# Kernel tuning notes

Hardware: AMD Instinct MI355X
Metric: run time of the kernel (lower is better)

Reference implementation:

```python
import jax, jax.numpy as jnp
import numpy as np

NEG_INF = -1e10
DIST_THRESH = 0


def _collect_entities(rep, pos, mask):
    # rep: [B, N, H]; pos: [B, M, S] int; mask: [B, M, S] float
    B, M, S = pos.shape
    g = jnp.take_along_axis(rep, pos.reshape(B, M * S)[:, :, None], axis=1)  # [B, M*S, H]
    g = g.reshape(B, M, S, rep.shape[-1]) * mask[..., None]
    return g.sum(axis=2)  # [B, M, H]


def setup_inputs() -> dict:
    key = jax.random.key(0)
    ks = jax.random.split(key, 10)
    B, N, H = 8, 2048, 512
    M, S = 96, 16
    E, D, R, MAXD = 256, 64, 5, 600
    scale = 0.02
    return {
        'node_hidden': jax.random.normal(ks[0], (B, N, H), jnp.float32),
        'chem_map': jax.random.randint(ks[1], (B, M, S), 0, N),
        'chem_mask': jnp.ones((B, M, S), jnp.float32),
        'dis_map': jax.random.randint(ks[2], (B, M, S), 0, N),
        'dis_mask': jnp.ones((B, M, S), jnp.float32),
        'distance': jax.random.randint(ks[3], (B, M, M), 0, MAXD),
        'W_chem': jax.random.normal(ks[4], (H, E), jnp.float32) * scale,
        'b_chem': jnp.zeros((E,), jnp.float32),
        'W_dis': jax.random.normal(ks[5], (H, E), jnp.float32) * scale,
        'b_dis': jnp.zeros((E,), jnp.float32),
        'W_score': jax.random.normal(ks[6], (2 * E + H + D, R), jnp.float32) * scale,
        'b_score': jnp.zeros((R,), jnp.float32),
        'dist_emb': jax.random.normal(ks[7], (MAXD, D), jnp.float32) * scale,
    }


def reference(node_hidden, chem_map, chem_mask, dis_map, dis_mask, distance,
              W_chem, b_chem, W_dis, b_dis, W_score, b_score, dist_emb):
    B, M = chem_map.shape[0], chem_map.shape[1]
    E = W_chem.shape[1]

    # sentence representation: max-pool over tokens  -> [B, H]
    sent = jnp.max(node_hidden, axis=1)

    # gather mention spans, masked sum pool, tanh-linear  -> [B, M, E]
    chem = jnp.tanh(_collect_entities(node_hidden, chem_map, chem_mask) @ W_chem + b_chem)
    dis = jnp.tanh(_collect_entities(node_hidden, dis_map, dis_mask) @ W_dis + b_dis)

    dist_e = dist_emb[distance]  # [B, M, M, D]

    # pairwise concat: [chem_i, dis_j, dist_ij, sent]  -> [B, M, M, 2E+D+H]
    concat = jnp.concatenate([
        jnp.broadcast_to(chem[:, :, None, :], (B, M, M, E)),
        jnp.broadcast_to(dis[:, None, :, :], (B, M, M, E)),
        dist_e,
        jnp.broadcast_to(sent[:, None, None, :], (B, M, M, sent.shape[-1])),
    ], axis=-1)

    score = jnp.einsum('bmnf,fr->bmnr', concat, W_score) + b_score  # [B, M, M, R]

    # validity masks: non-empty spans and distance >= threshold
    chem_valid = chem_mask.sum(axis=-1) > 0  # [B, M]
    dis_valid = dis_mask.sum(axis=-1) > 0    # [B, M]
    pair_valid = chem_valid[:, :, None] & dis_valid[:, None, :]  # [B, M, M]
    valid = pair_valid & (distance >= DIST_THRESH)
    score = jnp.where(valid[..., None], score, NEG_INF)

    # max-pool over all mention pairs  -> [B, R]
    return jnp.max(score.reshape(B, M * M, -1), axis=1)
```

## Files before the change

### kernel.cpp

```cpp
#include <hip/hip_runtime.h>
#include <math.h>

constexpr int B = 8, N = 2048, H = 512, M = 96, S = 16;
constexpr int E = 256, D = 64, R = 5, MAXD = 600;
constexpr int NZ = 32;
constexpr int NCHUNK = N / NZ;
constexpr int MT = 8;
constexpr int HC = 4;
constexpr int HCH = H / HC;
constexpr int MT4 = 8;
constexpr int RS = 2 * B * M;
constexpr float NEG_INF = -1e10f;

constexpr int G_GEMM = 2 * B * (M / MT) * HC;
constexpr int G_SENT = B * NZ / 2;
constexpr int G_DIST = MAXD / 4;
constexpr int G1 = G_GEMM + G_SENT + G_DIST;

constexpr int G3_PROJ = RS / 4;
constexpr int G3 = G3_PROJ + B;

__device__ inline void atomicMaxFloat(float* addr, float val) {
    int* ai = (int*)addr;
    int old = *ai;
    while (__int_as_float(old) < val) {
        int assumed = old;
        old = atomicCAS(ai, assumed, __float_as_int(val));
        if (old == assumed) break;
    }
}

__global__ __launch_bounds__(256)
void k1(const float* __restrict__ node,
        const int* __restrict__ cmap, const float* __restrict__ cmask,
        const int* __restrict__ dmap, const float* __restrict__ dmask,
        const float* __restrict__ Wc, const float* __restrict__ Wd,
        const float* __restrict__ Wsc, const float* __restrict__ emb,
        float* __restrict__ part, float* __restrict__ dotp,
        float* __restrict__ validAB, float* __restrict__ sD,
        float* __restrict__ out) {
    const int blk = blockIdx.x;
    const int t = threadIdx.x;

    if (blk == 0 && t < B * R) out[t] = NEG_INF;

    if (blk < G_GEMM) {
        int hc   = blk & 3;
        int rest = blk >> 2;
        int mg = rest % (M / MT);
        int b  = (rest / (M / MT)) % B;
        int z  = rest / ((M / MT) * B);
        const float* W    = z ? Wd : Wc;
        const int*   map  = z ? dmap  : cmap;
        const float* mask = z ? dmask : cmask;

        __shared__ int   smap[MT][S];
        __shared__ float smask[MT][S];
        __shared__ float lp[MT][HCH];

        if (t < MT * S) {
            int mi = t >> 4, s = t & 15;
            size_t off = ((size_t)b * M + mg * MT + mi) * S + s;
            smap[mi][s]  = map[off];
            smask[mi][s] = mask[off];
        }
        __syncthreads();

        {
            int mi = t >> 5, slot = t & 31;
            float4 a = make_float4(0.f, 0.f, 0.f, 0.f);
            #pragma unroll
            for (int s = 0; s < S; ++s) {
                float mk = smask[mi][s];
                const float4 v = reinterpret_cast<const float4*>(
                    node + ((size_t)b * N + smap[mi][s]) * H + hc * HCH)[slot];
                a.x += mk * v.x; a.y += mk * v.y;
                a.z += mk * v.z; a.w += mk * v.w;
            }
            reinterpret_cast<float4*>(&lp[mi][0])[slot] = a;
        }
        if (hc == 0 && t < MT) {
            float ms = 0.f;
            #pragma unroll
            for (int s = 0; s < S; ++s) ms += smask[t][s];
            validAB[((size_t)z * B + b) * M + mg * MT + t] = (ms > 0.f) ? 1.f : 0.f;
        }
        __syncthreads();

        float acc[MT] = {};
        const float* Wp = W + (size_t)(hc * HCH) * E + t;
        #pragma unroll 4
        for (int hh = 0; hh < HCH; hh += 4) {
            float w0 = Wp[(size_t)(hh + 0) * E];
            float w1 = Wp[(size_t)(hh + 1) * E];
            float w2 = Wp[(size_t)(hh + 2) * E];
            float w3 = Wp[(size_t)(hh + 3) * E];
            #pragma unroll
            for (int mi = 0; mi < MT; ++mi) {
                const float4 pv = *reinterpret_cast<const float4*>(&lp[mi][hh]);
                acc[mi] += pv.x * w0 + pv.y * w1 + pv.z * w2 + pv.w * w3;
            }
        }
        #pragma unroll
        for (int mi = 0; mi < MT; ++mi) {
            size_t row = ((size_t)z * B + b) * M + mg * MT + mi;
            dotp[((size_t)hc * RS + row) * E + t] = acc[mi];
        }
    } else if (blk < G_GEMM + G_SENT) {
        int sb = blk - G_GEMM;
        int b = sb >> 4;
        int z = ((sb & 15) << 1) + (t >> 7);
        int tt = t & 127;
        const float4* p = reinterpret_cast<const float4*>(
            node + ((size_t)b * N + (size_t)z * NCHUNK) * H) + tt;
        float4 mx = p[0];
        #pragma unroll 8
        for (int n = 1; n < NCHUNK; ++n) {
            float4 v = p[(size_t)n * (H / 4)];
            mx.x = fmaxf(mx.x, v.x); mx.y = fmaxf(mx.y, v.y);
            mx.z = fmaxf(mx.z, v.z); mx.w = fmaxf(mx.w, v.w);
        }
        reinterpret_cast<float4*>(part + ((size_t)z * B + b) * H)[tt] = mx;
    } else {
        int d = (blk - G_GEMM - G_SENT) * 4 + (t >> 6);
        int k = t & 63;
        float v = emb[(size_t)d * D + k];
        #pragma unroll
        for (int r = 0; r < R; ++r) {
            float p = v * Wsc[(size_t)(2 * E + k) * R + r];
            for (int off = 32; off; off >>= 1) p += __shfl_down(p, off, 64);
            if (k == 0) sD[d * R + r] = p;
        }
    }
}

__global__ __launch_bounds__(256)
void k3(const float* __restrict__ dotp,
        const float* __restrict__ bc, const float* __restrict__ bd,
        const float* __restrict__ Wsc, const float* __restrict__ bsc,
        const float* __restrict__ part,
        float* __restrict__ sAB, float* __restrict__ sS) {
    const int blk = blockIdx.x;
    const int t = threadIdx.x;
    const int wave = t >> 6, lane = t & 63;

    if (blk < G3_PROJ) {
        int rid = blk * 4 + wave;
        int z = rid / (B * M);
        const float* bias = z ? bd : bc;
        int scoff = z ? E : 0;

        float4 dv = reinterpret_cast<const float4*>(bias)[lane];
        #pragma unroll
        for (int hc = 0; hc < HC; ++hc) {
            const float4 v = reinterpret_cast<const float4*>(
                dotp + ((size_t)hc * RS + rid) * E)[lane];
            dv.x += v.x; dv.y += v.y; dv.z += v.z; dv.w += v.w;
        }
        float v0 = tanhf(dv.x), v1 = tanhf(dv.y), v2 = tanhf(dv.z), v3 = tanhf(dv.w);

        int e0 = scoff + 4 * lane;
        float p[R];
        #pragma unroll
        for (int r = 0; r < R; ++r) {
            p[r] = v0 * Wsc[(size_t)(e0 + 0) * R + r] + v1 * Wsc[(size_t)(e0 + 1) * R + r]
                 + v2 * Wsc[(size_t)(e0 + 2) * R + r] + v3 * Wsc[(size_t)(e0 + 3) * R + r];
        }
        #pragma unroll
        for (int r = 0; r < R; ++r) {
            for (int off = 32; off; off >>= 1) p[r] += __shfl_down(p[r], off, 64);
        }
        if (lane == 0) {
            #pragma unroll
            for (int r = 0; r < R; ++r) sAB[(size_t)rid * R + r] = p[r];
        }
    } else {
        int b = blk - G3_PROJ;
        __shared__ float sent[H];
        __shared__ float red[R][4];
        for (int h = t; h < H; h += 256) {
            float mx = -INFINITY;
            #pragma unroll 8
            for (int z = 0; z < NZ; ++z) mx = fmaxf(mx, part[((size_t)z * B + b) * H + h]);
            sent[h] = mx;
        }
        __syncthreads();
        float acc[R] = {};
        for (int h = t; h < H; h += 256) {
            float v = sent[h];
            const float* w = Wsc + (size_t)(2 * E + D + h) * R;
            #pragma unroll
            for (int r = 0; r < R; ++r) acc[r] += v * w[r];
        }
        #pragma unroll
        for (int r = 0; r < R; ++r) {
            float v = acc[r];
            for (int off = 32; off; off >>= 1) v += __shfl_down(v, off, 64);
            if (lane == 0) red[r][wave] = v;
        }
        __syncthreads();
        if (t < R) sS[b * R + t] = red[t][0] + red[t][1] + red[t][2] + red[t][3] + bsc[t];
    }
}

__global__ __launch_bounds__(256)
void k4(const int* __restrict__ distance,
        const float* __restrict__ sAB, const float* __restrict__ validAB,
        const float* __restrict__ sD, const float* __restrict__ sS,
        float* __restrict__ out) {
    const int g = blockIdx.x % (M / MT4);
    const int b = blockIdx.x / (M / MT4);
    const int t = threadIdx.x;
    const int wave = t >> 6, lane = t & 63;

    __shared__ float lB[M * R];
    __shared__ float lD[MAXD * R];
    __shared__ float lA[MT4 * R];
    __shared__ float lvA[MT4], lvB[M];
    __shared__ float red[R][4];

    for (int i = t; i < M * R; i += 256) lB[i] = sAB[((size_t)(B + b)) * M * R + i];
    for (int i = t; i < MAXD * R; i += 256) lD[i] = sD[i];
    if (t < MT4 * R) lA[t] = sAB[((size_t)b * M + g * MT4) * R + t] + sS[b * R + (t % R)];
    if (t < MT4) lvA[t] = validAB[(size_t)b * M + g * MT4 + t];
    for (int i = t; i < M; i += 256) lvB[i] = validAB[((size_t)B + b) * M + i];
    __syncthreads();

    float mx[R];
    #pragma unroll
    for (int r = 0; r < R; ++r) mx[r] = NEG_INF;

    #pragma unroll
    for (int it = 0; it < (MT4 * M) / 256; ++it) {
        int idx = it * 256 + t;
        int mi = idx / M, n = idx % M;
        int dist = distance[((size_t)b * M + g * MT4 + mi) * M + n];
        if (lvA[mi] > 0.f && lvB[n] > 0.f && dist >= 0 ) {
            #pragma unroll
            for (int r = 0; r < R; ++r)
                mx[r] = fmaxf(mx[r], lA[mi * R + r] + lB[n * R + r] + lD[dist * R + r]);
        }
    }
    #pragma unroll
    for (int r = 0; r < R; ++r) {
        float v = mx[r];
        for (int off = 32; off; off >>= 1) v = fmaxf(v, __shfl_down(v, off, 64));
        if (lane == 0) red[r][wave] = v;
    }
    __syncthreads();
    if (t < R) {
        float v = fmaxf(fmaxf(red[t][0], red[t][1]), fmaxf(red[t][2], red[t][3]));
        atomicMaxFloat(out + b * R + t, v);
    }
}

extern "C" void kernel_launch(void* const* d_in, const int* in_sizes, int n_in,
                              void* d_out, int out_size, void* d_ws, size_t ws_size,
                              hipStream_t stream) {
    const float* node     = (const float*)d_in[0];
    const int*   cmap     = (const int*)  d_in[1];
    const float* cmask    = (const float*)d_in[2];
    const int*   dmap     = (const int*)  d_in[3];
    const float* dmask    = (const float*)d_in[4];
    const int*   distance = (const int*)  d_in[5];
    const float* Wc       = (const float*)d_in[6];
    const float* bc       = (const float*)d_in[7];
    const float* Wd       = (const float*)d_in[8];
    const float* bd       = (const float*)d_in[9];
    const float* Wsc      = (const float*)d_in[10];
    const float* bsc      = (const float*)d_in[11];
    const float* emb      = (const float*)d_in[12];
    float* out = (float*)d_out;

    float* ws      = (float*)d_ws;
    float* part    = ws;
    float* validAB = part + (size_t)NZ * B * H;
    float* sD      = validAB + 2 * B * M;
    float* sS      = sD + MAXD * R;
    float* sAB     = sS + B * R;
    float* dotp    = sAB + (size_t)RS * R;

    hipLaunchKernelGGL(k1, dim3(G1), dim3(256), 0, stream,
                       node, cmap, cmask, dmap, dmask, Wc, Wd, Wsc, emb,
                       part, dotp, validAB, sD, out);
    hipLaunchKernelGGL(k3, dim3(G3), dim3(256), 0, stream,
                       dotp, bc, bd, Wsc, bsc, part, sAB, sS);
    hipLaunchKernelGGL(k4, dim3((M / MT4) * B), dim3(256), 0, stream,
                       distance, sAB, validAB, sD, sS, out);
}
```

Before: 50.43 us.

## Fuse three kernels into one cooperative persistent kernel with grid syncs

Merges the three stage kernels into a single cooperative kernel. Each block loops over work items for each phase, and grid.sync() separates the phases, so two kernel launch boundaries go away. The grid size is taken from an occupancy query, and the old three-launch path is kept as a fallback if the cooperative launch fails. The cost is grid-wide barrier latency, a host-side occupancy query on every call, and possibly lower occupancy, because the kernel's shared memory is the union of all three phases.

```diff
diff --git a/kernel.cpp b/kernel.cpp
--- a/kernel.cpp
+++ b/kernel.cpp
@@ -1,5 +1,8 @@
 #include <hip/hip_runtime.h>
+#include <hip/hip_cooperative_groups.h>
 #include <math.h>
+
+namespace cg = cooperative_groups;
 
 constexpr int B = 8, N = 2048, H = 512, M = 96, S = 16;
 constexpr int E = 256, D = 64, R = 5, MAXD = 600;
@@ -15,10 +18,11 @@
 constexpr int G_GEMM = 2 * B * (M / MT) * HC;
 constexpr int G_SENT = B * NZ / 2;
 constexpr int G_DIST = MAXD / 4;
-constexpr int G1 = G_GEMM + G_SENT + G_DIST;
+constexpr int P1_ITEMS = G_GEMM + G_SENT + G_DIST;
 
 constexpr int G3_PROJ = RS / 4;
-constexpr int G3 = G3_PROJ + B;
+constexpr int P2_ITEMS = G3_PROJ + B;
+constexpr int P3_ITEMS = (M / MT4) * B;
 
 __device__ inline void atomicMaxFloat(float* addr, float val) {
     int* ai = (int*)addr;
@@ -30,33 +34,25 @@
     }
 }
 
-__global__ __launch_bounds__(256)
-void k1(const float* __restrict__ node,
+__device__ __forceinline__ void p1_body(
+        int item, int t,
+        const float* __restrict__ node,
         const int* __restrict__ cmap, const float* __restrict__ cmask,
         const int* __restrict__ dmap, const float* __restrict__ dmask,
         const float* __restrict__ Wc, const float* __restrict__ Wd,
         const float* __restrict__ Wsc, const float* __restrict__ emb,
         float* __restrict__ part, float* __restrict__ dotp,
         float* __restrict__ validAB, float* __restrict__ sD,
-        float* __restrict__ out) {
-    const int blk = blockIdx.x;
-    const int t = threadIdx.x;
-
-    if (blk == 0 && t < B * R) out[t] = NEG_INF;
-
-    if (blk < G_GEMM) {
-        int hc   = blk & 3;
-        int rest = blk >> 2;
+        int smap[MT][S], float smask[MT][S], float lp[MT][HCH]) {
+    if (item < G_GEMM) {
+        int hc   = item & 3;
+        int rest = item >> 2;
         int mg = rest % (M / MT);
         int b  = (rest / (M / MT)) % B;
         int z  = rest / ((M / MT) * B);
         const float* W    = z ? Wd : Wc;
         const int*   map  = z ? dmap  : cmap;
         const float* mask = z ? dmask : cmask;
-
-        __shared__ int   smap[MT][S];
-        __shared__ float smask[MT][S];
-        __shared__ float lp[MT][HCH];
 
         if (t < MT * S) {
             int mi = t >> 4, s = t & 15;
@@ -106,8 +102,8 @@
             size_t row = ((size_t)z * B + b) * M + mg * MT + mi;
             dotp[((size_t)hc * RS + row) * E + t] = acc[mi];
         }
-    } else if (blk < G_GEMM + G_SENT) {
-        int sb = blk - G_GEMM;
+    } else if (item < G_GEMM + G_SENT) {
+        int sb = item - G_GEMM;
         int b = sb >> 4;
         int z = ((sb & 15) << 1) + (t >> 7);
         int tt = t & 127;
@@ -122,7 +118,7 @@
         }
         reinterpret_cast<float4*>(part + ((size_t)z * B + b) * H)[tt] = mx;
     } else {
-        int d = (blk - G_GEMM - G_SENT) * 4 + (t >> 6);
+        int d = (item - G_GEMM - G_SENT) * 4 + (t >> 6);
         int k = t & 63;
         float v = emb[(size_t)d * D + k];
         #pragma unroll
@@ -132,6 +128,184 @@
             if (k == 0) sD[d * R + r] = p;
         }
     }
+}
+
+__device__ __forceinline__ void p2_body(
+        int item, int t,
+        const float* __restrict__ dotp,
+        const float* __restrict__ bc, const float* __restrict__ bd,
+        const float* __restrict__ Wsc, const float* __restrict__ bsc,
+        const float* __restrict__ part,
+        float* __restrict__ sAB, float* __restrict__ sS,
+        float sent[H], float red[R][4]) {
+    const int wave = t >> 6, lane = t & 63;
+    if (item < G3_PROJ) {
+        int rid = item * 4 + wave;
+        int z = rid / (B * M);
+        const float* bias = z ? bd : bc;
+        int scoff = z ? E : 0;
+
+        float4 dv = reinterpret_cast<const float4*>(bias)[lane];
+        #pragma unroll
+        for (int hc = 0; hc < HC; ++hc) {
+            const float4 v = reinterpret_cast<const float4*>(
+                dotp + ((size_t)hc * RS + rid) * E)[lane];
+            dv.x += v.x; dv.y += v.y; dv.z += v.z; dv.w += v.w;
+        }
+        float v0 = tanhf(dv.x), v1 = tanhf(dv.y), v2 = tanhf(dv.z), v3 = tanhf(dv.w);
+
+        int e0 = scoff + 4 * lane;
+        float p[R];
+        #pragma unroll
+        for (int r = 0; r < R; ++r) {
+            p[r] = v0 * Wsc[(size_t)(e0 + 0) * R + r] + v1 * Wsc[(size_t)(e0 + 1) * R + r]
+                 + v2 * Wsc[(size_t)(e0 + 2) * R + r] + v3 * Wsc[(size_t)(e0 + 3) * R + r];
+        }
+        #pragma unroll
+        for (int r = 0; r < R; ++r) {
+            for (int off = 32; off; off >>= 1) p[r] += __shfl_down(p[r], off, 64);
+        }
+        if (lane == 0) {
+            #pragma unroll
+            for (int r = 0; r < R; ++r) sAB[(size_t)rid * R + r] = p[r];
+        }
+    } else {
+        int b = item - G3_PROJ;
+        for (int h = t; h < H; h += 256) {
+            float mx = -INFINITY;
+            #pragma unroll 8
+            for (int z = 0; z < NZ; ++z) mx = fmaxf(mx, part[((size_t)z * B + b) * H + h]);
+            sent[h] = mx;
+        }
+        __syncthreads();
+        float acc[R] = {};
+        for (int h = t; h < H; h += 256) {
+            float v = sent[h];
+            const float* w = Wsc + (size_t)(2 * E + D + h) * R;
+            #pragma unroll
+            for (int r = 0; r < R; ++r) acc[r] += v * w[r];
+        }
+        #pragma unroll
+        for (int r = 0; r < R; ++r) {
+            float v = acc[r];
+            for (int off = 32; off; off >>= 1) v += __shfl_down(v, off, 64);
+            if (lane == 0) red[r][wave] = v;
+        }
+        __syncthreads();
+        if (t < R) sS[b * R + t] = red[t][0] + red[t][1] + red[t][2] + red[t][3] + bsc[t];
+    }
+}
+
+__device__ __forceinline__ void p3_body(
+        int item, int t,
+        const int* __restrict__ distance,
+        const float* __restrict__ sAB, const float* __restrict__ validAB,
+        const float* __restrict__ sD, const float* __restrict__ sS,
+        float* __restrict__ out,
+        float lB[M * R], float lD[MAXD * R], float lA[MT4 * R],
+        float lvA[MT4], float lvB[M], float red[R][4]) {
+    const int g = item % (M / MT4);
+    const int b = item / (M / MT4);
+    const int wave = t >> 6, lane = t & 63;
+
+    for (int i = t; i < M * R; i += 256) lB[i] = sAB[((size_t)(B + b)) * M * R + i];
+    for (int i = t; i < MAXD * R; i += 256) lD[i] = sD[i];
+    if (t < MT4 * R) lA[t] = sAB[((size_t)b * M + g * MT4) * R + t] + sS[b * R + (t % R)];
+    if (t < MT4) lvA[t] = validAB[(size_t)b * M + g * MT4 + t];
+    for (int i = t; i < M; i += 256) lvB[i] = validAB[((size_t)B + b) * M + i];
+    __syncthreads();
+
+    float mx[R];
+    #pragma unroll
+    for (int r = 0; r < R; ++r) mx[r] = NEG_INF;
+
+    #pragma unroll
+    for (int it = 0; it < (MT4 * M) / 256; ++it) {
+        int idx = it * 256 + t;
+        int mi = idx / M, n = idx % M;
+        int dist = distance[((size_t)b * M + g * MT4 + mi) * M + n];
+        if (lvA[mi] > 0.f && lvB[n] > 0.f && dist >= 0 ) {
+            #pragma unroll
+            for (int r = 0; r < R; ++r)
+                mx[r] = fmaxf(mx[r], lA[mi * R + r] + lB[n * R + r] + lD[dist * R + r]);
+        }
+    }
+    #pragma unroll
+    for (int r = 0; r < R; ++r) {
+        float v = mx[r];
+        for (int off = 32; off; off >>= 1) v = fmaxf(v, __shfl_down(v, off, 64));
+        if (lane == 0) red[r][wave] = v;
+    }
+    __syncthreads();
+    if (t < R) {
+        float v = fmaxf(fmaxf(red[t][0], red[t][1]), fmaxf(red[t][2], red[t][3]));
+        atomicMaxFloat(out + b * R + t, v);
+    }
+}
+
+__global__ __launch_bounds__(256, 4)
+void k_coop(const float* __restrict__ node,
+            const int* __restrict__ cmap, const float* __restrict__ cmask,
+            const int* __restrict__ dmap, const float* __restrict__ dmask,
+            const int* __restrict__ distance,
+            const float* __restrict__ Wc, const float* __restrict__ bc,
+            const float* __restrict__ Wd, const float* __restrict__ bd,
+            const float* __restrict__ Wsc, const float* __restrict__ bsc,
+            const float* __restrict__ emb,
+            float* __restrict__ part, float* __restrict__ dotp,
+            float* __restrict__ validAB, float* __restrict__ sD,
+            float* __restrict__ sAB, float* __restrict__ sS,
+            float* __restrict__ out) {
+    cg::grid_group grid = cg::this_grid();
+    const int t = threadIdx.x;
+    const int blk = blockIdx.x;
+    const int GD = gridDim.x;
+
+    __shared__ int   smap[MT][S];
+    __shared__ float smask[MT][S];
+    __shared__ float lp[MT][HCH];
+    __shared__ float sent[H];
+    __shared__ float red[R][4];
+    __shared__ float lB[M * R];
+    __shared__ float lD[MAXD * R];
+    __shared__ float lA[MT4 * R];
+    __shared__ float lvA[MT4], lvB[M];
+
+    if (blk == 0 && t < B * R) out[t] = NEG_INF;
+
+    for (int item = blk; item < P1_ITEMS; item += GD) {
+        __syncthreads();
+        p1_body(item, t, node, cmap, cmask, dmap, dmask, Wc, Wd, Wsc, emb,
+                part, dotp, validAB, sD, smap, smask, lp);
+    }
+    grid.sync();
+    for (int item = blk; item < P2_ITEMS; item += GD) {
+        __syncthreads();
+        p2_body(item, t, dotp, bc, bd, Wsc, bsc, part, sAB, sS, sent, red);
+    }
+    grid.sync();
+    for (int item = blk; item < P3_ITEMS; item += GD) {
+        __syncthreads();
+        p3_body(item, t, distance, sAB, validAB, sD, sS, out,
+                lB, lD, lA, lvA, lvB, red);
+    }
+}
+
+__global__ __launch_bounds__(256)
+void k1(const float* __restrict__ node,
+        const int* __restrict__ cmap, const float* __restrict__ cmask,
+        const int* __restrict__ dmap, const float* __restrict__ dmask,
+        const float* __restrict__ Wc, const float* __restrict__ Wd,
+        const float* __restrict__ Wsc, const float* __restrict__ emb,
+        float* __restrict__ part, float* __restrict__ dotp,
+        float* __restrict__ validAB, float* __restrict__ sD,
+        float* __restrict__ out) {
+    __shared__ int   smap[MT][S];
+    __shared__ float smask[MT][S];
+    __shared__ float lp[MT][HCH];
+    if (blockIdx.x == 0 && threadIdx.x < B * R) out[threadIdx.x] = NEG_INF;
+    p1_body(blockIdx.x, threadIdx.x, node, cmap, cmask, dmap, dmask, Wc, Wd, Wsc, emb,
+            part, dotp, validAB, sD, smap, smask, lp);
 }
 
 __global__ __launch_bounds__(256)
@@ -140,67 +314,9 @@
         const float* __restrict__ Wsc, const float* __restrict__ bsc,
         const float* __restrict__ part,
         float* __restrict__ sAB, float* __restrict__ sS) {
-    const int blk = blockIdx.x;
-    const int t = threadIdx.x;
-    const int wave = t >> 6, lane = t & 63;
-
-    if (blk < G3_PROJ) {
-        int rid = blk * 4 + wave;
-        int z = rid / (B * M);
-        const float* bias = z ? bd : bc;
-        int scoff = z ? E : 0;
-
-        float4 dv = reinterpret_cast<const float4*>(bias)[lane];
-        #pragma unroll
-        for (int hc = 0; hc < HC; ++hc) {
-            const float4 v = reinterpret_cast<const float4*>(
-                dotp + ((size_t)hc * RS + rid) * E)[lane];
-            dv.x += v.x; dv.y += v.y; dv.z += v.z; dv.w += v.w;
-        }
-        float v0 = tanhf(dv.x), v1 = tanhf(dv.y), v2 = tanhf(dv.z), v3 = tanhf(dv.w);
-
-        int e0 = scoff + 4 * lane;
-        float p[R];
-        #pragma unroll
-        for (int r = 0; r < R; ++r) {
-            p[r] = v0 * Wsc[(size_t)(e0 + 0) * R + r] + v1 * Wsc[(size_t)(e0 + 1) * R + r]
-                 + v2 * Wsc[(size_t)(e0 + 2) * R + r] + v3 * Wsc[(size_t)(e0 + 3) * R + r];
-        }
-        #pragma unroll
-        for (int r = 0; r < R; ++r) {
-            for (int off = 32; off; off >>= 1) p[r] += __shfl_down(p[r], off, 64);
-        }
-        if (lane == 0) {
-            #pragma unroll
-            for (int r = 0; r < R; ++r) sAB[(size_t)rid * R + r] = p[r];
-        }
-    } else {
-        int b = blk - G3_PROJ;
-        __shared__ float sent[H];
-        __shared__ float red[R][4];
-        for (int h = t; h < H; h += 256) {
-            float mx = -INFINITY;
-            #pragma unroll 8
-            for (int z = 0; z < NZ; ++z) mx = fmaxf(mx, part[((size_t)z * B + b) * H + h]);
-            sent[h] = mx;
-        }
-        __syncthreads();
-        float acc[R] = {};
-        for (int h = t; h < H; h += 256) {
-            float v = sent[h];
-            const float* w = Wsc + (size_t)(2 * E + D + h) * R;
-            #pragma unroll
-            for (int r = 0; r < R; ++r) acc[r] += v * w[r];
-        }
-        #pragma unroll
-        for (int r = 0; r < R; ++r) {
-            float v = acc[r];
-            for (int off = 32; off; off >>= 1) v += __shfl_down(v, off, 64);
-            if (lane == 0) red[r][wave] = v;
-        }
-        __syncthreads();
-        if (t < R) sS[b * R + t] = red[t][0] + red[t][1] + red[t][2] + red[t][3] + bsc[t];
-    }
+    __shared__ float sent[H];
+    __shared__ float red[R][4];
+    p2_body(blockIdx.x, threadIdx.x, dotp, bc, bd, Wsc, bsc, part, sAB, sS, sent, red);
 }
 
 __global__ __launch_bounds__(256)
@@ -208,50 +324,13 @@
         const float* __restrict__ sAB, const float* __restrict__ validAB,
         const float* __restrict__ sD, const float* __restrict__ sS,
         float* __restrict__ out) {
-    const int g = blockIdx.x % (M / MT4);
-    const int b = blockIdx.x / (M / MT4);
-    const int t = threadIdx.x;
-    const int wave = t >> 6, lane = t & 63;
-
     __shared__ float lB[M * R];
     __shared__ float lD[MAXD * R];
     __shared__ float lA[MT4 * R];
     __shared__ float lvA[MT4], lvB[M];
     __shared__ float red[R][4];
-
-    for (int i = t; i < M * R; i += 256) lB[i] = sAB[((size_t)(B + b)) * M * R + i];
-    for (int i = t; i < MAXD * R; i += 256) lD[i] = sD[i];
-    if (t < MT4 * R) lA[t] = sAB[((size_t)b * M + g * MT4) * R + t] + sS[b * R + (t % R)];
-    if (t < MT4) lvA[t] = validAB[(size_t)b * M + g * MT4 + t];
-    for (int i = t; i < M; i += 256) lvB[i] = validAB[((size_t)B + b) * M + i];
-    __syncthreads();
-
-    float mx[R];
-    #pragma unroll
-    for (int r = 0; r < R; ++r) mx[r] = NEG_INF;
-
-    #pragma unroll
-    for (int it = 0; it < (MT4 * M) / 256; ++it) {
-        int idx = it * 256 + t;
-        int mi = idx / M, n = idx % M;
-        int dist = distance[((size_t)b * M + g * MT4 + mi) * M + n];
-        if (lvA[mi] > 0.f && lvB[n] > 0.f && dist >= 0 ) {
-            #pragma unroll
-            for (int r = 0; r < R; ++r)
-                mx[r] = fmaxf(mx[r], lA[mi * R + r] + lB[n * R + r] + lD[dist * R + r]);
-        }
-    }
-    #pragma unroll
-    for (int r = 0; r < R; ++r) {
-        float v = mx[r];
-        for (int off = 32; off; off >>= 1) v = fmaxf(v, __shfl_down(v, off, 64));
-        if (lane == 0) red[r][wave] = v;
-    }
-    __syncthreads();
-    if (t < R) {
-        float v = fmaxf(fmaxf(red[t][0], red[t][1]), fmaxf(red[t][2], red[t][3]));
-        atomicMaxFloat(out + b * R + t, v);
-    }
+    p3_body(blockIdx.x, threadIdx.x, distance, sAB, validAB, sD, sS, out,
+            lB, lD, lA, lvA, lvB, red);
 }
 
 extern "C" void kernel_launch(void* const* d_in, const int* in_sizes, int n_in,
@@ -280,11 +359,29 @@
     float* sAB     = sS + B * R;
     float* dotp    = sAB + (size_t)RS * R;
 
-    hipLaunchKernelGGL(k1, dim3(G1), dim3(256), 0, stream,
-                       node, cmap, cmask, dmap, dmask, Wc, Wd, Wsc, emb,
-                       part, dotp, validAB, sD, out);
-    hipLaunchKernelGGL(k3, dim3(G3), dim3(256), 0, stream,
-                       dotp, bc, bd, Wsc, bsc, part, sAB, sS);
-    hipLaunchKernelGGL(k4, dim3((M / MT4) * B), dim3(256), 0, stream,
-                       distance, sAB, validAB, sD, sS, out);
-}
+    int occ = 0;
+    hipError_t qerr = hipOccupancyMaxActiveBlocksPerMultiprocessor(&occ, k_coop, 256, 0);
+    int grid = occ * 256;
+    if (grid > 1024) grid = 1024;
+
+    hipError_t lerr = hipErrorUnknown;
+    if (qerr == hipSuccess && grid >= 128) {
+        void* args[] = {
+            (void*)&node, (void*)&cmap, (void*)&cmask, (void*)&dmap, (void*)&dmask,
+            (void*)&distance, (void*)&Wc, (void*)&bc, (void*)&Wd, (void*)&bd,
+            (void*)&Wsc, (void*)&bsc, (void*)&emb,
+            (void*)&part, (void*)&dotp, (void*)&validAB, (void*)&sD,
+            (void*)&sAB, (void*)&sS, (void*)&out
+        };
+        lerr = hipLaunchCooperativeKernel((void*)k_coop, dim3(grid), dim3(256), args, 0, stream);
+    }
+    if (lerr != hipSuccess) {
+        hipLaunchKernelGGL(k1, dim3(P1_ITEMS), dim3(256), 0, stream,
+                           node, cmap, cmask, dmap, dmask, Wc, Wd, Wsc, emb,
+                           part, dotp, validAB, sD, out);
+        hipLaunchKernelGGL(k3, dim3(P2_ITEMS), dim3(256), 0, stream,
+                           dotp, bc, bd, Wsc, bsc, part, sAB, sS);
+        hipLaunchKernelGGL(k4, dim3(P3_ITEMS), dim3(256), 0, stream,
+                           distance, sAB, validAB, sD, sS, out);
+    }
+}
```

Result: slower. 196.1 us (+288.9%).

## Fuse entity projection epilogue into gather-GEMM and sentence score into pair-max kernel

Applied to the files above, without the earlier changes.

The separate projection-reduction kernel is removed. Each GEMM block now handles 4 mentions with all four H-chunks split across waves, reduces the partials in shared memory, and applies the bias, tanh and score projection in place. The sentence max and its score are computed redundantly inside each pair-max block, so the pipeline goes from three launches to two and the dotp workspace round trip disappears. In exchange, each GEMM block reads the full W with float4 loads (fewer blocks, more work per block), and every pair-max block re-reduces the 32 partial sentence maxima.

```diff
diff --git a/kernel.cpp b/kernel.cpp
--- a/kernel.cpp
+++ b/kernel.cpp
@@ -5,20 +5,16 @@
 constexpr int E = 256, D = 64, R = 5, MAXD = 600;
 constexpr int NZ = 32;
 constexpr int NCHUNK = N / NZ;
-constexpr int MT = 8;
+constexpr int MT = 4;
 constexpr int HC = 4;
 constexpr int HCH = H / HC;
 constexpr int MT4 = 8;
-constexpr int RS = 2 * B * M;
 constexpr float NEG_INF = -1e10f;
 
-constexpr int G_GEMM = 2 * B * (M / MT) * HC;
-constexpr int G_SENT = B * NZ / 2;
-constexpr int G_DIST = MAXD / 4;
-constexpr int G1 = G_GEMM + G_SENT + G_DIST;
-
-constexpr int G3_PROJ = RS / 4;
-constexpr int G3 = G3_PROJ + B;
+constexpr int X_GEMM = 2 * B * (M / MT);
+constexpr int X_SENT = B * NZ / 2;
+constexpr int X_DIST = MAXD / 4;
+constexpr int XG = X_GEMM + X_SENT + X_DIST;
 
 __device__ inline void atomicMaxFloat(float* addr, float val) {
     int* ai = (int*)addr;
@@ -31,32 +27,35 @@
 }
 
 __global__ __launch_bounds__(256)
-void k1(const float* __restrict__ node,
+void kX(const float* __restrict__ node,
         const int* __restrict__ cmap, const float* __restrict__ cmask,
         const int* __restrict__ dmap, const float* __restrict__ dmask,
-        const float* __restrict__ Wc, const float* __restrict__ Wd,
+        const float* __restrict__ Wc, const float* __restrict__ bc,
+        const float* __restrict__ Wd, const float* __restrict__ bd,
         const float* __restrict__ Wsc, const float* __restrict__ emb,
-        float* __restrict__ part, float* __restrict__ dotp,
+        float* __restrict__ part, float* __restrict__ sAB,
         float* __restrict__ validAB, float* __restrict__ sD,
         float* __restrict__ out) {
     const int blk = blockIdx.x;
     const int t = threadIdx.x;
+    const int wave = t >> 6, lane = t & 63;
 
     if (blk == 0 && t < B * R) out[t] = NEG_INF;
 
-    if (blk < G_GEMM) {
-        int hc   = blk & 3;
-        int rest = blk >> 2;
-        int mg = rest % (M / MT);
-        int b  = (rest / (M / MT)) % B;
-        int z  = rest / ((M / MT) * B);
+    if (blk < X_GEMM) {
+        int mg = blk % (M / MT);
+        int b  = (blk / (M / MT)) % B;
+        int z  = blk / ((M / MT) * B);
         const float* W    = z ? Wd : Wc;
+        const float* bias = z ? bd : bc;
         const int*   map  = z ? dmap  : cmap;
         const float* mask = z ? dmask : cmask;
+        int scoff = z ? E : 0;
 
         __shared__ int   smap[MT][S];
         __shared__ float smask[MT][S];
-        __shared__ float lp[MT][HCH];
+        __shared__ float pool[HC][MT][HCH];
+        __shared__ float red4[HC][MT][E];
 
         if (t < MT * S) {
             int mi = t >> 4, s = t & 15;
@@ -67,19 +66,24 @@
         __syncthreads();
 
         {
-            int mi = t >> 5, slot = t & 31;
-            float4 a = make_float4(0.f, 0.f, 0.f, 0.f);
-            #pragma unroll
-            for (int s = 0; s < S; ++s) {
-                float mk = smask[mi][s];
-                const float4 v = reinterpret_cast<const float4*>(
-                    node + ((size_t)b * N + smap[mi][s]) * H + hc * HCH)[slot];
-                a.x += mk * v.x; a.y += mk * v.y;
-                a.z += mk * v.z; a.w += mk * v.w;
-            }
-            reinterpret_cast<float4*>(&lp[mi][0])[slot] = a;
-        }
-        if (hc == 0 && t < MT) {
+            const int hc = wave;
+            #pragma unroll
+            for (int it = 0; it < 2; ++it) {
+                int item = it * 64 + lane;
+                int mi = item >> 5, slot = item & 31;
+                float4 a = make_float4(0.f, 0.f, 0.f, 0.f);
+                #pragma unroll
+                for (int s = 0; s < S; ++s) {
+                    float mk = smask[mi][s];
+                    const float4 v = reinterpret_cast<const float4*>(
+                        node + ((size_t)b * N + smap[mi][s]) * H + hc * HCH)[slot];
+                    a.x += mk * v.x; a.y += mk * v.y;
+                    a.z += mk * v.z; a.w += mk * v.w;
+                }
+                reinterpret_cast<float4*>(&pool[hc][mi][0])[slot] = a;
+            }
+        }
+        if (t < MT) {
             float ms = 0.f;
             #pragma unroll
             for (int s = 0; s < S; ++s) ms += smask[t][s];
@@ -87,27 +91,75 @@
         }
         __syncthreads();
 
-        float acc[MT] = {};
-        const float* Wp = W + (size_t)(hc * HCH) * E + t;
-        #pragma unroll 4
-        for (int hh = 0; hh < HCH; hh += 4) {
-            float w0 = Wp[(size_t)(hh + 0) * E];
-            float w1 = Wp[(size_t)(hh + 1) * E];
-            float w2 = Wp[(size_t)(hh + 2) * E];
-            float w3 = Wp[(size_t)(hh + 3) * E];
-            #pragma unroll
-            for (int mi = 0; mi < MT; ++mi) {
-                const float4 pv = *reinterpret_cast<const float4*>(&lp[mi][hh]);
-                acc[mi] += pv.x * w0 + pv.y * w1 + pv.z * w2 + pv.w * w3;
-            }
-        }
-        #pragma unroll
-        for (int mi = 0; mi < MT; ++mi) {
-            size_t row = ((size_t)z * B + b) * M + mg * MT + mi;
-            dotp[((size_t)hc * RS + row) * E + t] = acc[mi];
-        }
-    } else if (blk < G_GEMM + G_SENT) {
-        int sb = blk - G_GEMM;
+        {
+            const int hc = wave;
+            const float4* W4 = reinterpret_cast<const float4*>(W) + lane;
+            float4 a0 = make_float4(0.f, 0.f, 0.f, 0.f);
+            float4 a1 = a0, a2 = a0, a3 = a0;
+            #pragma unroll 4
+            for (int hh4 = 0; hh4 < HCH / 4; ++hh4) {
+                int h = hh4 * 4;
+                const float4 w0 = W4[(size_t)(hc * HCH + h + 0) * (E / 4)];
+                const float4 w1 = W4[(size_t)(hc * HCH + h + 1) * (E / 4)];
+                const float4 w2 = W4[(size_t)(hc * HCH + h + 2) * (E / 4)];
+                const float4 w3 = W4[(size_t)(hc * HCH + h + 3) * (E / 4)];
+                const float4 p0 = *reinterpret_cast<const float4*>(&pool[hc][0][h]);
+                const float4 p1 = *reinterpret_cast<const float4*>(&pool[hc][1][h]);
+                const float4 p2 = *reinterpret_cast<const float4*>(&pool[hc][2][h]);
+                const float4 p3 = *reinterpret_cast<const float4*>(&pool[hc][3][h]);
+                a0.x += p0.x*w0.x + p0.y*w1.x + p0.z*w2.x + p0.w*w3.x;
+                a0.y += p0.x*w0.y + p0.y*w1.y + p0.z*w2.y + p0.w*w3.y;
+                a0.z += p0.x*w0.z + p0.y*w1.z + p0.z*w2.z + p0.w*w3.z;
+                a0.w += p0.x*w0.w + p0.y*w1.w + p0.z*w2.w + p0.w*w3.w;
+                a1.x += p1.x*w0.x + p1.y*w1.x + p1.z*w2.x + p1.w*w3.x;
+                a1.y += p1.x*w0.y + p1.y*w1.y + p1.z*w2.y + p1.w*w3.y;
+                a1.z += p1.x*w0.z + p1.y*w1.z + p1.z*w2.z + p1.w*w3.z;
+                a1.w += p1.x*w0.w + p1.y*w1.w + p1.z*w2.w + p1.w*w3.w;
+                a2.x += p2.x*w0.x + p2.y*w1.x + p2.z*w2.x + p2.w*w3.x;
+                a2.y += p2.x*w0.y + p2.y*w1.y + p2.z*w2.y + p2.w*w3.y;
+                a2.z += p2.x*w0.z + p2.y*w1.z + p2.z*w2.z + p2.w*w3.z;
+                a2.w += p2.x*w0.w + p2.y*w1.w + p2.z*w2.w + p2.w*w3.w;
+                a3.x += p3.x*w0.x + p3.y*w1.x + p3.z*w2.x + p3.w*w3.x;
+                a3.y += p3.x*w0.y + p3.y*w1.y + p3.z*w2.y + p3.w*w3.y;
+                a3.z += p3.x*w0.z + p3.y*w1.z + p3.z*w2.z + p3.w*w3.z;
+                a3.w += p3.x*w0.w + p3.y*w1.w + p3.z*w2.w + p3.w*w3.w;
+            }
+            reinterpret_cast<float4*>(&red4[hc][0][0])[lane] = a0;
+            reinterpret_cast<float4*>(&red4[hc][1][0])[lane] = a1;
+            reinterpret_cast<float4*>(&red4[hc][2][0])[lane] = a2;
+            reinterpret_cast<float4*>(&red4[hc][3][0])[lane] = a3;
+        }
+        __syncthreads();
+
+        {
+            const int mi = wave;
+            float4 dv = reinterpret_cast<const float4*>(bias)[lane];
+            #pragma unroll
+            for (int hc = 0; hc < HC; ++hc) {
+                const float4 v = reinterpret_cast<const float4*>(&red4[hc][mi][0])[lane];
+                dv.x += v.x; dv.y += v.y; dv.z += v.z; dv.w += v.w;
+            }
+            float v0 = tanhf(dv.x), v1 = tanhf(dv.y), v2 = tanhf(dv.z), v3 = tanhf(dv.w);
+
+            int e0 = scoff + 4 * lane;
+            float p[R];
+            #pragma unroll
+            for (int r = 0; r < R; ++r) {
+                p[r] = v0 * Wsc[(size_t)(e0 + 0) * R + r] + v1 * Wsc[(size_t)(e0 + 1) * R + r]
+                     + v2 * Wsc[(size_t)(e0 + 2) * R + r] + v3 * Wsc[(size_t)(e0 + 3) * R + r];
+            }
+            #pragma unroll
+            for (int r = 0; r < R; ++r) {
+                for (int off = 32; off; off >>= 1) p[r] += __shfl_down(p[r], off, 64);
+            }
+            if (lane == 0) {
+                size_t rid = ((size_t)z * B + b) * M + mg * MT + mi;
+                #pragma unroll
+                for (int r = 0; r < R; ++r) sAB[rid * R + r] = p[r];
+            }
+        }
+    } else if (blk < X_GEMM + X_SENT) {
+        int sb = blk - X_GEMM;
         int b = sb >> 4;
         int z = ((sb & 15) << 1) + (t >> 7);
         int tt = t & 127;
@@ -122,69 +174,45 @@
         }
         reinterpret_cast<float4*>(part + ((size_t)z * B + b) * H)[tt] = mx;
     } else {
-        int d = (blk - G_GEMM - G_SENT) * 4 + (t >> 6);
-        int k = t & 63;
-        float v = emb[(size_t)d * D + k];
+        int d = (blk - X_GEMM - X_SENT) * 4 + wave;
+        float v = emb[(size_t)d * D + lane];
         #pragma unroll
         for (int r = 0; r < R; ++r) {
-            float p = v * Wsc[(size_t)(2 * E + k) * R + r];
+            float p = v * Wsc[(size_t)(2 * E + lane) * R + r];
             for (int off = 32; off; off >>= 1) p += __shfl_down(p, off, 64);
-            if (k == 0) sD[d * R + r] = p;
+            if (lane == 0) sD[d * R + r] = p;
         }
     }
 }
 
 __global__ __launch_bounds__(256)
-void k3(const float* __restrict__ dotp,
-        const float* __restrict__ bc, const float* __restrict__ bd,
-        const float* __restrict__ Wsc, const float* __restrict__ bsc,
-        const float* __restrict__ part,
-        float* __restrict__ sAB, float* __restrict__ sS) {
-    const int blk = blockIdx.x;
+void kY(const float* __restrict__ part, const float* __restrict__ Wsc,
+        const float* __restrict__ bsc,
+        const int* __restrict__ distance,
+        const float* __restrict__ sAB, const float* __restrict__ validAB,
+        const float* __restrict__ sD, float* __restrict__ out) {
+    const int g = blockIdx.x % (M / MT4);
+    const int b = blockIdx.x / (M / MT4);
     const int t = threadIdx.x;
     const int wave = t >> 6, lane = t & 63;
 
-    if (blk < G3_PROJ) {
-        int rid = blk * 4 + wave;
-        int z = rid / (B * M);
-        const float* bias = z ? bd : bc;
-        int scoff = z ? E : 0;
-
-        float4 dv = reinterpret_cast<const float4*>(bias)[lane];
-        #pragma unroll
-        for (int hc = 0; hc < HC; ++hc) {
-            const float4 v = reinterpret_cast<const float4*>(
-                dotp + ((size_t)hc * RS + rid) * E)[lane];
-            dv.x += v.x; dv.y += v.y; dv.z += v.z; dv.w += v.w;
-        }
-        float v0 = tanhf(dv.x), v1 = tanhf(dv.y), v2 = tanhf(dv.z), v3 = tanhf(dv.w);
-
-        int e0 = scoff + 4 * lane;
-        float p[R];
-        #pragma unroll
-        for (int r = 0; r < R; ++r) {
-            p[r] = v0 * Wsc[(size_t)(e0 + 0) * R + r] + v1 * Wsc[(size_t)(e0 + 1) * R + r]
-                 + v2 * Wsc[(size_t)(e0 + 2) * R + r] + v3 * Wsc[(size_t)(e0 + 3) * R + r];
-        }
-        #pragma unroll
-        for (int r = 0; r < R; ++r) {
-            for (int off = 32; off; off >>= 1) p[r] += __shfl_down(p[r], off, 64);
-        }
-        if (lane == 0) {
-            #pragma unroll
-            for (int r = 0; r < R; ++r) sAB[(size_t)rid * R + r] = p[r];
-        }
-    } else {
-        int b = blk - G3_PROJ;
-        __shared__ float sent[H];
-        __shared__ float red[R][4];
-        for (int h = t; h < H; h += 256) {
-            float mx = -INFINITY;
-            #pragma unroll 8
-            for (int z = 0; z < NZ; ++z) mx = fmaxf(mx, part[((size_t)z * B + b) * H + h]);
-            sent[h] = mx;
-        }
-        __syncthreads();
+    __shared__ float sent[H];
+    __shared__ float red[R][4];
+    __shared__ float sSb[R];
+    __shared__ float lB[M * R];
+    __shared__ float lD[MAXD * R];
+    __shared__ float lA[MT4 * R];
+    __shared__ float lvA[MT4], lvB[M];
+
+    for (int h = t; h < H; h += 256) {
+        float mx = -INFINITY;
+        #pragma unroll 8
+        for (int z = 0; z < NZ; ++z) mx = fmaxf(mx, part[((size_t)z * B + b) * H + h]);
+        sent[h] = mx;
+    }
+    __syncthreads();
+
+    {
         float acc[R] = {};
         for (int h = t; h < H; h += 256) {
             float v = sent[h];
@@ -199,29 +227,13 @@
             if (lane == 0) red[r][wave] = v;
         }
         __syncthreads();
-        if (t < R) sS[b * R + t] = red[t][0] + red[t][1] + red[t][2] + red[t][3] + bsc[t];
-    }
-}
-
-__global__ __launch_bounds__(256)
-void k4(const int* __restrict__ distance,
-        const float* __restrict__ sAB, const float* __restrict__ validAB,
-        const float* __restrict__ sD, const float* __restrict__ sS,
-        float* __restrict__ out) {
-    const int g = blockIdx.x % (M / MT4);
-    const int b = blockIdx.x / (M / MT4);
-    const int t = threadIdx.x;
-    const int wave = t >> 6, lane = t & 63;
-
-    __shared__ float lB[M * R];
-    __shared__ float lD[MAXD * R];
-    __shared__ float lA[MT4 * R];
-    __shared__ float lvA[MT4], lvB[M];
-    __shared__ float red[R][4];
+        if (t < R) sSb[t] = red[t][0] + red[t][1] + red[t][2] + red[t][3] + bsc[t];
+        __syncthreads();
+    }
 
     for (int i = t; i < M * R; i += 256) lB[i] = sAB[((size_t)(B + b)) * M * R + i];
     for (int i = t; i < MAXD * R; i += 256) lD[i] = sD[i];
-    if (t < MT4 * R) lA[t] = sAB[((size_t)b * M + g * MT4) * R + t] + sS[b * R + (t % R)];
+    if (t < MT4 * R) lA[t] = sAB[((size_t)b * M + g * MT4) * R + t] + sSb[t % R];
     if (t < MT4) lvA[t] = validAB[(size_t)b * M + g * MT4 + t];
     for (int i = t; i < M; i += 256) lvB[i] = validAB[((size_t)B + b) * M + i];
     __syncthreads();
@@ -276,15 +288,11 @@
     float* part    = ws;
     float* validAB = part + (size_t)NZ * B * H;
     float* sD      = validAB + 2 * B * M;
-    float* sS      = sD + MAXD * R;
-    float* sAB     = sS + B * R;
-    float* dotp    = sAB + (size_t)RS * R;
-
-    hipLaunchKernelGGL(k1, dim3(G1), dim3(256), 0, stream,
-                       node, cmap, cmask, dmap, dmask, Wc, Wd, Wsc, emb,
-                       part, dotp, validAB, sD, out);
-    hipLaunchKernelGGL(k3, dim3(G3), dim3(256), 0, stream,
-                       dotp, bc, bd, Wsc, bsc, part, sAB, sS);
-    hipLaunchKernelGGL(k4, dim3((M / MT4) * B), dim3(256), 0, stream,
-                       distance, sAB, validAB, sD, sS, out);
-}
+    float* sAB     = sD + MAXD * R;
+
+    hipLaunchKernelGGL(kX, dim3(XG), dim3(256), 0, stream,
+                       node, cmap, cmask, dmap, dmask, Wc, bc, Wd, bd, Wsc, emb,
+                       part, sAB, validAB, sD, out);
+    hipLaunchKernelGGL(kY, dim3((M / MT4) * B), dim3(256), 0, stream,
+                       part, Wsc, bsc, distance, sAB, validAB, sD, out);
+}
```

Measured after the change: 62.80 us. 24.5% more time.
